# Kernel tuning notes

Measured on AMD Instinct MI355X. Metric: run time of the kernel, lower is better.

The kernel has to match this reference:

```python
import jax, jax.numpy as jnp
import numpy as np

N_NODES = 50000
N_REL = 8
D_IN = 64      # review_dim (in_feats)
D_OUT = 32     # attention_feats (final_dim)
H = 2          # num_heads
N_EDGES = 800000
NEG_SLOPE = 0.2


def gather_mm(x, w, b, idx):
    """Per-edge relation-indexed GEMM: out[e] = x[e] @ w[idx[e]] + b[idx[e]].
    Loops over the small fixed relation set (R=8) instead of materializing
    an [E, D, HF] gathered weight tensor."""
    out = jnp.zeros((x.shape[0], w.shape[-1]), dtype=x.dtype)
    for r in range(w.shape[0]):
        out = out + jnp.where((idx == r)[:, None], x @ w[r] + b[r], jnp.zeros((), x.dtype))
    return out


def setup_inputs() -> dict:
    key = jax.random.key(0)
    ks = jax.random.split(key, 11)
    feat = jax.random.normal(ks[0], (N_NODES, D_IN), dtype=jnp.float32)
    src = jax.random.randint(ks[1], (N_EDGES,), 0, N_NODES)
    dst = jax.random.randint(ks[2], (N_EDGES,), 0, N_NODES)
    r_type = jax.random.randint(ks[3], (N_EDGES,), 0, N_REL)
    nid = jax.random.randint(ks[4], (N_EDGES,), 0, N_NODES)
    fc_src = jax.random.normal(ks[5], (N_REL, D_IN, H * D_OUT), dtype=jnp.float32) * 0.1
    fc_src_bias = jax.random.normal(ks[6], (N_REL, H * D_OUT), dtype=jnp.float32) * 0.1
    node_quality = jax.random.normal(ks[7], (N_NODES, D_IN), dtype=jnp.float32)
    fc_qual = jax.random.normal(ks[8], (N_REL, D_IN, H * D_OUT), dtype=jnp.float32) * 0.1
    fc_qual_bias = jax.random.normal(ks[9], (N_REL, H * D_OUT), dtype=jnp.float32) * 0.1
    attn = jax.random.normal(ks[10], (N_REL, H, D_OUT), dtype=jnp.float32) * 0.1
    return {"feat": feat, "src": src, "dst": dst, "r_type": r_type, "nid": nid,
            "fc_src": fc_src, "fc_src_bias": fc_src_bias, "node_quality": node_quality,
            "fc_qual": fc_qual, "fc_qual_bias": fc_qual_bias, "attn": attn}


def reference(feat, src, dst, r_type, nid, fc_src, fc_src_bias,
              node_quality, fc_qual, fc_qual_bias, attn):
    E = src.shape[0]
    h_src = feat  # feat_drop is identity (p=0)

    # el: relation-aware projection of source features, per edge -> [E, H, D_OUT]
    el = gather_mm(h_src[src], fc_src, fc_src_bias, r_type).reshape(E, H, D_OUT)
    # qual: relation-aware projection of per-edge node-quality embedding
    h_qual = node_quality[nid]
    qual = gather_mm(h_qual, fc_qual, fc_qual_bias, r_type).reshape(E, H, D_OUT)

    # additive attention logits, relation-indexed attn vector -> [E, H]
    e = jax.nn.leaky_relu(el + qual, negative_slope=NEG_SLOPE)
    e = jnp.sum(e * attn[r_type], axis=-1)  # [E, H]

    # edge_softmax over incoming edges of each dst node (per head)
    emax = jax.ops.segment_max(e, dst, num_segments=N_NODES)  # [N, H]
    emax = jnp.where(jnp.isfinite(emax), emax, jnp.zeros((), e.dtype))
    ex = jnp.exp(e - emax[dst])
    denom = jax.ops.segment_sum(ex, dst, num_segments=N_NODES)
    a = ex / denom[dst]  # [E, H]

    # NARRE: messages are raw source features weighted by attention
    msg = h_src[src][:, None, :] * a[:, :, None]  # [E, H, D_IN]
    rst = jax.ops.segment_sum(msg, dst, num_segments=N_NODES)  # [N, H, D_IN]
    return rst
```

## Files before the change

kernel.cpp:

```cpp
#include <hip/hip_runtime.h>
#include <hip/hip_bf16.h>

#define NN 50000
#define NR 8
#define NE 800000
#define NBLK_E 3125
#define NWV (NBLK_E * 4)
#define NCH 13

typedef short bf16x8 __attribute__((ext_vector_type(8)));
typedef float f32x4  __attribute__((ext_vector_type(4)));

__device__ __forceinline__ unsigned fkey(float f) {
    unsigned b = __float_as_uint(f);
    return (b & 0x80000000u) ? ~b : (b | 0x80000000u);
}
__device__ __forceinline__ float funkey(unsigned k) {
    unsigned b = (k & 0x80000000u) ? (k ^ 0x80000000u) : ~k;
    return __uint_as_float(b);
}
__device__ __forceinline__ unsigned short f2bf(float f) {
    unsigned u = __float_as_uint(f);
    unsigned r = (u + 0x7FFFu + ((u >> 16) & 1u)) >> 16;
    return (unsigned short)r;
}
__device__ __forceinline__ float bf2f(unsigned short b) {
    return __uint_as_float(((unsigned)b) << 16);
}

__global__ __launch_bounds__(256) void conv_kernel(
    const float* __restrict__ feat, const float* __restrict__ nq,
    const float* __restrict__ WS, const float* __restrict__ WQ,
    const float* __restrict__ bS, const float* __restrict__ bQ,
    unsigned short* __restrict__ xS, unsigned short* __restrict__ xQ,
    unsigned short* __restrict__ WtS, unsigned short* __restrict__ WtQ,
    float* __restrict__ bSQ)
{
    const int idx = blockIdx.x * 256 + threadIdx.x;
    const int NX = NN * 64 / 4;
    if (idx < NX) {
        const float4 v = reinterpret_cast<const float4*>(feat)[idx];
        ushort4 p; p.x = f2bf(v.x); p.y = f2bf(v.y); p.z = f2bf(v.z); p.w = f2bf(v.w);
        reinterpret_cast<ushort4*>(xS)[idx] = p;
    } else if (idx < 2 * NX) {
        const float4 v = reinterpret_cast<const float4*>(nq)[idx - NX];
        ushort4 p; p.x = f2bf(v.x); p.y = f2bf(v.y); p.z = f2bf(v.z); p.w = f2bf(v.w);
        reinterpret_cast<ushort4*>(xQ)[idx - NX] = p;
    } else {
        int i = idx - 2 * NX;
        if (i < 32768) {
            const int r = i >> 12, rem = i & 4095, o = rem >> 6, k = rem & 63;
            WtS[i] = f2bf(WS[(size_t)r * 4096 + k * 64 + o]);
        } else if (i < 65536) {
            i -= 32768;
            const int r = i >> 12, rem = i & 4095, o = rem >> 6, k = rem & 63;
            WtQ[i] = f2bf(WQ[(size_t)r * 4096 + k * 64 + o]);
        } else if (i < 65536 + 512) {
            const int j = i - 65536;
            bSQ[j] = bS[j] + bQ[j];
        }
    }
}

__global__ __launch_bounds__(256) void hist_kernel(
    const int* __restrict__ dst, const int* __restrict__ rt,
    int* __restrict__ cnt, int* __restrict__ rank, int* __restrict__ rhist)
{
    const int t = threadIdx.x, e = blockIdx.x * 256 + t;
    const int w = t >> 6, lane = t & 63;
    const int d = dst[e], r = rt[e];
    rank[e] = atomicAdd(&cnt[d], 1);
    #pragma unroll
    for (int rr = 0; rr < 8; ++rr) {
        const unsigned long long m = __ballot(r == rr);
        if (lane == 0) rhist[rr * NWV + blockIdx.x * 4 + w] = __popcll(m);
    }
}

__global__ __launch_bounds__(256) void scanrb1_kernel(
    const int* __restrict__ rhist, int* __restrict__ rbase0, int* __restrict__ psum)
{
    __shared__ int s[256];
    __shared__ int carry;
    const int c = blockIdx.x, r = blockIdx.y, t = threadIdx.x;
    if (t == 0) carry = 0;
    __syncthreads();
    const int i1 = min((c + 1) * 1024, NWV);
    for (int b0 = c * 1024; b0 < i1; b0 += 256) {
        const int i = b0 + t;
        const int v = (i < i1) ? rhist[r * NWV + i] : 0;
        s[t] = v;
        __syncthreads();
        #pragma unroll
        for (int off = 1; off < 256; off <<= 1) {
            const int x = (t >= off) ? s[t - off] : 0;
            __syncthreads();
            s[t] += x;
            __syncthreads();
        }
        if (i < i1) rbase0[r * NWV + i] = carry + s[t] - v;
        __syncthreads();
        if (t == 0) carry += s[255];
        __syncthreads();
    }
    if (t == 0) psum[r * NCH + c] = carry;
}

__global__ __launch_bounds__(256) void scan1_kernel(
    const int* __restrict__ cnt, int* __restrict__ offs, int* __restrict__ partial)
{
    __shared__ int s[256];
    const int t = threadIdx.x, i = blockIdx.x * 256 + t;
    const int v = (i < NN) ? cnt[i] : 0;
    s[t] = v;
    __syncthreads();
    #pragma unroll
    for (int off = 1; off < 256; off <<= 1) {
        const int x = (t >= off) ? s[t - off] : 0;
        __syncthreads();
        s[t] += x;
        __syncthreads();
    }
    if (i < NN) offs[i] = s[t] - v;
    if (t == 255) partial[blockIdx.x] = s[255];
}

__global__ __launch_bounds__(256) void scan2_kernel(
    int* __restrict__ partial, const int nblk,
    const int* __restrict__ psum, int* __restrict__ off_pad,
    int* __restrict__ cbase, int4* __restrict__ meta)
{
    __shared__ int s[256];
    __shared__ int sop[9];
    __shared__ int scr[8];
    const int t = threadIdx.x;
    const int v = (t < nblk) ? partial[t] : 0;
    s[t] = v;
    __syncthreads();
    #pragma unroll
    for (int off = 1; off < 256; off <<= 1) {
        const int x = (t >= off) ? s[t - off] : 0;
        __syncthreads();
        s[t] += x;
        __syncthreads();
    }
    if (t < nblk) partial[t] = s[t] - v;
    if (t == 0) {
        int cr[8];
        for (int r = 0; r < NR; ++r) {
            cr[r] = 0;
            for (int c = 0; c < NCH; ++c) cr[r] += psum[r * NCH + c];
        }
        int acc = 0;
        for (int r = 0; r < NR; ++r) {
            sop[r] = acc; off_pad[r] = acc; scr[r] = cr[r];
            int a2 = acc;
            for (int c = 0; c < NCH; ++c) { cbase[r * NCH + c] = a2; a2 += psum[r * NCH + c]; }
            acc += (cr[r] + 255) & ~255;
        }
        sop[8] = acc; off_pad[8] = acc;
    }
    __syncthreads();
    for (int r = 0; r < NR; ++r) {
        const int s0 = sop[r] + scr[r], s1 = sop[r + 1];
        for (int i = s0 + t; i < s1; i += 256) meta[i] = make_int4(0, 0, -1, 0);
    }
}

__global__ __launch_bounds__(256) void scan3_kernel(
    int* __restrict__ offs, const int* __restrict__ partial)
{
    const int i = blockIdx.x * 256 + threadIdx.x;
    if (i < NN) offs[i] += partial[blockIdx.x];
    if (i == 0) offs[NN] = NE;
}

__global__ __launch_bounds__(256) void fillr_kernel(
    const int* __restrict__ rt, const int* __restrict__ src,
    const int* __restrict__ nid, const int* __restrict__ dst,
    const int* __restrict__ offs, const int* __restrict__ rank,
    const int* __restrict__ rbase0, const int* __restrict__ cbase,
    int4* __restrict__ meta)
{
    const int t = threadIdx.x, e = blockIdx.x * 256 + t;
    const int w = t >> 6, lane = t & 63;
    const int r = rt[e];
    unsigned long long mymask = 0;
    #pragma unroll
    for (int rr = 0; rr < 8; ++rr) {
        const unsigned long long m = __ballot(r == rr);
        if (r == rr) mymask = m;
    }
    const int rk = (int)__popcll(mymask & ((1ull << lane) - 1ull));
    const int wv = blockIdx.x * 4 + w;
    const int slot = cbase[r * NCH + (wv >> 10)] + rbase0[r * NWV + wv] + rk;
    const int j = offs[dst[e]] + rank[e];
    meta[slot] = make_int4(src[e], nid[e], j, 0);
}

__global__ __launch_bounds__(256) void logits_kernel(
    const unsigned short* __restrict__ xS, const unsigned short* __restrict__ xQ,
    const unsigned short* __restrict__ WtS, const unsigned short* __restrict__ WtQ,
    const float* __restrict__ bSQ, const float* __restrict__ attn,
    const int4* __restrict__ meta, const int* __restrict__ off_pad,
    float4* __restrict__ perm)
{
    __shared__ bf16x8 ldsS[512];
    __shared__ bf16x8 ldsQ[512];
    const int slot0 = blockIdx.x * 256;
    int r = 0;
    #pragma unroll
    for (int i = 1; i <= 8; ++i) r += (slot0 >= off_pad[i]);
    if (r >= 8) return;

    const int t = threadIdx.x;
    for (int c = t; c < 512; c += 256) {
        const int row = c >> 3, c8 = c & 7, sw = c8 ^ (row & 7);
        ldsS[row * 8 + sw] = *reinterpret_cast<const bf16x8*>(WtS + (size_t)r * 4096 + c * 8);
        ldsQ[row * 8 + sw] = *reinterpret_cast<const bf16x8*>(WtQ + (size_t)r * 4096 + c * 8);
    }
    __syncthreads();

    const int lane = t & 63, l15 = lane & 15, g = lane >> 4, l7 = l15 & 7;
    const int sbase = slot0 + (t >> 6) * 64;

    int4 mt[4];
    #pragma unroll
    for (int b = 0; b < 4; ++b) mt[b] = meta[sbase + b * 16 + l15];

    bf16x8 xf[4][2], qf[4][2];
    #pragma unroll
    for (int b = 0; b < 4; ++b) {
        const unsigned short* xp = xS + (size_t)mt[b].x * 64;
        const unsigned short* qp = xQ + (size_t)mt[b].y * 64;
        xf[b][0] = *reinterpret_cast<const bf16x8*>(xp + g * 8);
        xf[b][1] = *reinterpret_cast<const bf16x8*>(xp + 32 + g * 8);
        qf[b][0] = *reinterpret_cast<const bf16x8*>(qp + g * 8);
        qf[b][1] = *reinterpret_cast<const bf16x8*>(qp + 32 + g * 8);
    }

    float p0[4] = {0.f, 0.f, 0.f, 0.f}, p1[4] = {0.f, 0.f, 0.f, 0.f};
    #pragma unroll
    for (int ot = 0; ot < 4; ++ot) {
        const int row8 = (ot * 16 + l15) * 8;
        const bf16x8 wS0 = ldsS[row8 + (g ^ l7)];
        const bf16x8 wS1 = ldsS[row8 + ((4 + g) ^ l7)];
        const bf16x8 wQ0 = ldsQ[row8 + (g ^ l7)];
        const bf16x8 wQ1 = ldsQ[row8 + ((4 + g) ^ l7)];
        const f32x4 bv = *reinterpret_cast<const f32x4*>(bSQ  + r * 64 + ot * 16 + g * 4);
        const f32x4 av = *reinterpret_cast<const f32x4*>(attn + r * 64 + ot * 16 + g * 4);
        #pragma unroll
        for (int b = 0; b < 4; ++b) {
            f32x4 acc = (f32x4){0.f, 0.f, 0.f, 0.f};
            acc = __builtin_amdgcn_mfma_f32_16x16x32_bf16(wS0, xf[b][0], acc, 0, 0, 0);
            acc = __builtin_amdgcn_mfma_f32_16x16x32_bf16(wS1, xf[b][1], acc, 0, 0, 0);
            acc = __builtin_amdgcn_mfma_f32_16x16x32_bf16(wQ0, qf[b][0], acc, 0, 0, 0);
            acc = __builtin_amdgcn_mfma_f32_16x16x32_bf16(wQ1, qf[b][1], acc, 0, 0, 0);
            float part = 0.f;
            #pragma unroll
            for (int j = 0; j < 4; ++j) {
                float v = acc[j] + bv[j];
                v = v > 0.f ? v : 0.2f * v;
                part += v * av[j];
            }
            if (ot < 2) p0[b] += part; else p1[b] += part;
        }
    }
    #pragma unroll
    for (int b = 0; b < 4; ++b) {
        p0[b] += __shfl_xor(p0[b], 16); p0[b] += __shfl_xor(p0[b], 32);
        p1[b] += __shfl_xor(p1[b], 16); p1[b] += __shfl_xor(p1[b], 32);
        if (g == 0 && mt[b].z >= 0)
            perm[mt[b].z] = make_float4(__int_as_float(mt[b].x), p0[b], p1[b], 0.f);
    }
}

__global__ __launch_bounds__(256) void aggregate_kernel(
    const unsigned short* __restrict__ xS, const int* __restrict__ offs,
    const float4* __restrict__ perm, float* __restrict__ out)
{
    __shared__ float2 ebuf[4][64];
    __shared__ int    sbuf[4][64];
    const int wv = threadIdx.x >> 6;
    const int n = blockIdx.x * 4 + wv;
    if (n >= NN) return;
    const int lane = threadIdx.x & 63;
    const int h2 = lane >> 5;
    const int dp = lane & 31;
    const int s0 = offs[n], s1 = offs[n + 1];
    float a00 = 0.f, a01 = 0.f, a10 = 0.f, a11 = 0.f;
    float d0s = 0.f, d1s = 0.f;
    if (s1 > s0) {
        float m0 = -1e30f, m1 = -1e30f;
        for (int j = s0 + lane; j < s1; j += 64) {
            const float4 p = perm[j];
            m0 = fmaxf(m0, p.y); m1 = fmaxf(m1, p.z);
        }
        #pragma unroll
        for (int m = 32; m; m >>= 1) {
            m0 = fmaxf(m0, __shfl_xor(m0, m));
            m1 = fmaxf(m1, __shfl_xor(m1, m));
        }
        for (int c = s0; c < s1; c += 64) {
            const int cnt = min(64, s1 - c);
            if (lane < cnt) {
                const float4 p = perm[c + lane];
                const float e0 = __expf(p.y - m0);
                const float e1 = __expf(p.z - m1);
                d0s += e0; d1s += e1;
                ebuf[wv][lane] = make_float2(e0, e1);
                sbuf[wv][lane] = (int)__float_as_uint(p.x);
            } else if (lane == cnt) {
                ebuf[wv][lane] = make_float2(0.f, 0.f);
                sbuf[wv][lane] = 0;
            }
            const int cp = cnt + (cnt & 1);
            #pragma unroll 4
            for (int k = 0; k < cp; k += 2) {
                const int ei = k + h2;
                const int sA = sbuf[wv][ei];
                const float2 w = ebuf[wv][ei];
                const unsigned fv = *reinterpret_cast<const unsigned*>(
                    xS + (size_t)sA * 64 + dp * 2);
                const float fx = bf2f((unsigned short)(fv & 0xFFFFu));
                const float fy = bf2f((unsigned short)(fv >> 16));
                a00 += fx * w.x; a01 += fy * w.x;
                a10 += fx * w.y; a11 += fy * w.y;
            }
        }
        #pragma unroll
        for (int m = 32; m; m >>= 1) {
            d0s += __shfl_xor(d0s, m);
            d1s += __shfl_xor(d1s, m);
        }
        a00 += __shfl_xor(a00, 32); a01 += __shfl_xor(a01, 32);
        a10 += __shfl_xor(a10, 32); a11 += __shfl_xor(a11, 32);
        const float r0 = 1.f / d0s, r1 = 1.f / d1s;
        a00 *= r0; a01 *= r0; a10 *= r1; a11 *= r1;
    }
    if (h2 == 0)
        *reinterpret_cast<float2*>(&out[(size_t)n * 128 + dp * 2])      = make_float2(a00, a01);
    else
        *reinterpret_cast<float2*>(&out[(size_t)n * 128 + 64 + dp * 2]) = make_float2(a10, a11);
}

__global__ __launch_bounds__(256) void logits_direct_kernel(
    const float* __restrict__ feat, const float* __restrict__ nq,
    const int* __restrict__ src, const int* __restrict__ dst,
    const int* __restrict__ rt, const int* __restrict__ nid,
    const float* __restrict__ fc_src, const float* __restrict__ fc_src_b,
    const float* __restrict__ fc_qual, const float* __restrict__ fc_qual_b,
    const float* __restrict__ attn,
    float* __restrict__ e_buf, unsigned* __restrict__ emax)
{
    __shared__ float Ws[64][64];
    __shared__ float Wq[64][64];
    __shared__ float bl[64];
    __shared__ float al[64];
    const int r = blockIdx.y;
    const int t = threadIdx.x;
    for (int i = t; i < 4096; i += 256) {
        ((float*)Ws)[i] = fc_src[(size_t)r * 4096 + i];
        ((float*)Wq)[i] = fc_qual[(size_t)r * 4096 + i];
    }
    if (t < 64) {
        bl[t] = fc_src_b[r * 64 + t] + fc_qual_b[r * 64 + t];
        al[t] = attn[r * 64 + t];
    }
    __syncthreads();

    const int lane = t & 63;
    const int wid = blockIdx.x * 4 + (t >> 6);
    const int nw = gridDim.x * 4;
    for (int e = wid; e < NE; e += nw) {
        if (rt[e] != r) continue;
        const int s = src[e], q = nid[e];
        float fv = feat[(size_t)s * 64 + lane];
        float qv = nq[(size_t)q * 64 + lane];
        float acc = bl[lane];
        for (int k = 0; k < 64; ++k) {
            acc += __shfl(fv, k) * Ws[k][lane];
            acc += __shfl(qv, k) * Wq[k][lane];
        }
        acc = acc > 0.f ? acc : 0.2f * acc;
        float p = acc * al[lane];
        #pragma unroll
        for (int m = 1; m < 32; m <<= 1) p += __shfl_xor(p, m);
        if ((lane & 31) == 0) {
            int h = lane >> 5;
            e_buf[(size_t)e * 2 + h] = p;
            atomicMax(&emax[(size_t)dst[e] * 2 + h], fkey(p));
        }
    }
}

__global__ __launch_bounds__(256) void expdenom_kernel(
    const int* __restrict__ dst, float* __restrict__ e_buf,
    const unsigned* __restrict__ emax, float* __restrict__ denom)
{
    const int i = blockIdx.x * 256 + threadIdx.x;
    if (i >= NE * 2) return;
    const int e = i >> 1, h = i & 1;
    const int dn = dst[e];
    const float m = funkey(emax[(size_t)dn * 2 + h]);
    const float ex = __expf(e_buf[i] - m);
    e_buf[i] = ex;
    unsafeAtomicAdd(&denom[(size_t)dn * 2 + h], ex);
}

__global__ __launch_bounds__(256) void scatter_kernel(
    const float* __restrict__ feat, const int* __restrict__ src, const int* __restrict__ dst,
    const float* __restrict__ ex, const float* __restrict__ denom, float* __restrict__ out)
{
    const int e = blockIdx.x * 4 + (threadIdx.x >> 6);
    if (e >= NE) return;
    const int lane = threadIdx.x & 63;
    const int s = src[e], dn = dst[e];
    const float f = feat[(size_t)s * 64 + lane];
    const float a0 = ex[(size_t)e * 2]     / denom[(size_t)dn * 2];
    const float a1 = ex[(size_t)e * 2 + 1] / denom[(size_t)dn * 2 + 1];
    unsafeAtomicAdd(&out[(size_t)dn * 128 + lane],      f * a0);
    unsafeAtomicAdd(&out[(size_t)dn * 128 + 64 + lane], f * a1);
}

extern "C" void kernel_launch(void* const* d_in, const int* in_sizes, int n_in,
                              void* d_out, int out_size, void* d_ws, size_t ws_size,
                              hipStream_t stream)
{
    const float* feat      = (const float*)d_in[0];
    const int*   src       = (const int*)d_in[1];
    const int*   dst       = (const int*)d_in[2];
    const int*   rt        = (const int*)d_in[3];
    const int*   nid       = (const int*)d_in[4];
    const float* fc_src    = (const float*)d_in[5];
    const float* fc_src_b  = (const float*)d_in[6];
    const float* nq        = (const float*)d_in[7];
    const float* fc_qual   = (const float*)d_in[8];
    const float* fc_qual_b = (const float*)d_in[9];
    const float* attn      = (const float*)d_in[10];
    float* out = (float*)d_out;

    char* ws = (char*)d_ws;

    int*    cnt      = (int*)ws;
    int*    offs     = (int*)(ws + 262144);
    int*    partial  = (int*)(ws + 524288);
    int*    off_pad  = (int*)(ws + 528384);
    int*    psum     = (int*)(ws + 528512);
    int*    cbase    = (int*)(ws + 528960);
    int*    rhist    = (int*)(ws + 655360);
    int*    rbase0   = (int*)(ws + 1055360);
    int*    rank     = (int*)(ws + 1455360);
    int4*   meta     = (int4*)(ws + 4718592);
    float4* perm     = (float4*)(ws + 17551360);
    unsigned short* xS  = (unsigned short*)(ws + 30351360);
    unsigned short* xQ  = (unsigned short*)(ws + 36751360);
    unsigned short* WtS = (unsigned short*)(ws + 43151360);
    unsigned short* WtQ = (unsigned short*)(ws + 43216896);
    float*          bSQ = (float*)(ws + 43282432);
    const size_t need = 43284480;

    if (ws_size >= need) {
        hipMemsetAsync(cnt, 0, 200000, stream);

        conv_kernel<<<6508, 256, 0, stream>>>(
            feat, nq, fc_src, fc_qual, fc_src_b, fc_qual_b, xS, xQ, WtS, WtQ, bSQ);
        hist_kernel<<<NBLK_E, 256, 0, stream>>>(dst, rt, cnt, rank, rhist);
        {
            dim3 g(NCH, NR);
            scanrb1_kernel<<<g, 256, 0, stream>>>(rhist, rbase0, psum);
        }

        const int nblk = (NN + 255) / 256;
        scan1_kernel<<<nblk, 256, 0, stream>>>(cnt, offs, partial);
        scan2_kernel<<<1, 256, 0, stream>>>(partial, nblk, psum, off_pad, cbase, meta);
        scan3_kernel<<<nblk, 256, 0, stream>>>(offs, partial);
        fillr_kernel<<<NBLK_E, 256, 0, stream>>>(
            rt, src, nid, dst, offs, rank, rbase0, cbase, meta);

        logits_kernel<<<(NE + 8 * 256) / 256, 256, 0, stream>>>(
            xS, xQ, WtS, WtQ, bSQ, attn, meta, off_pad, perm);
        aggregate_kernel<<<(NN + 3) / 4, 256, 0, stream>>>(xS, offs, perm, out);
    } else {
        float*    e_buf = (float*)ws;
        unsigned* emax  = (unsigned*)(ws + (size_t)NE * 2 * 4);
        float*    denom = (float*)(ws + (size_t)NE * 2 * 4 + (size_t)NN * 2 * 4);
        hipMemsetAsync(out, 0, (size_t)out_size * sizeof(float), stream);
        hipMemsetAsync(emax, 0, (size_t)NN * 2 * 4 * 2, stream);
        dim3 g(256, NR);
        logits_direct_kernel<<<g, 256, 0, stream>>>(
            feat, nq, src, dst, rt, nid, fc_src, fc_src_b, fc_qual, fc_qual_b,
            attn, e_buf, emax);
        expdenom_kernel<<<(NE * 2 + 255) / 256, 256, 0, stream>>>(dst, e_buf, emax, denom);
        scatter_kernel<<<(NE + 3) / 4, 256, 0, stream>>>(feat, src, dst, e_buf, denom, out);
    }
}
```

Measured before the change: 160.8 us.

## Fuse conversion with histogram, compress logits to bf16, prefetch weights to registers

Merges the bf16 conversion kernel and the dst/relation histogram kernel into one launch, removing a kernel launch and its gap. The per-edge logits record shrinks from a float4 to a uint2 holding the source index plus two bf16-packed logits, halving perm traffic between the logits and aggregate kernels. In the logits kernel, weight tiles are loaded into registers before the gathers and written to LDS afterwards, so global weight loads overlap the feature gathers. Storing logits in bf16 lowers softmax precision and may affect accuracy.

```diff
diff --git a/kernel.cpp b/kernel.cpp
--- a/kernel.cpp
+++ b/kernel.cpp
@@ -28,15 +28,19 @@
     return __uint_as_float(((unsigned)b) << 16);
 }
 
-__global__ __launch_bounds__(256) void conv_kernel(
+__global__ __launch_bounds__(256) void conv_hist_kernel(
     const float* __restrict__ feat, const float* __restrict__ nq,
     const float* __restrict__ WS, const float* __restrict__ WQ,
     const float* __restrict__ bS, const float* __restrict__ bQ,
+    const int* __restrict__ dst, const int* __restrict__ rt,
     unsigned short* __restrict__ xS, unsigned short* __restrict__ xQ,
     unsigned short* __restrict__ WtS, unsigned short* __restrict__ WtQ,
-    float* __restrict__ bSQ)
-{
-    const int idx = blockIdx.x * 256 + threadIdx.x;
+    float* __restrict__ bSQ,
+    int* __restrict__ cnt, int* __restrict__ rank, int* __restrict__ rhist)
+{
+    const int t = threadIdx.x;
+    const int idx = blockIdx.x * 256 + t;
+
     const int NX = NN * 64 / 4;
     if (idx < NX) {
         const float4 v = reinterpret_cast<const float4*>(feat)[idx];
@@ -60,20 +64,16 @@
             bSQ[j] = bS[j] + bQ[j];
         }
     }
-}
-
-__global__ __launch_bounds__(256) void hist_kernel(
-    const int* __restrict__ dst, const int* __restrict__ rt,
-    int* __restrict__ cnt, int* __restrict__ rank, int* __restrict__ rhist)
-{
-    const int t = threadIdx.x, e = blockIdx.x * 256 + t;
-    const int w = t >> 6, lane = t & 63;
-    const int d = dst[e], r = rt[e];
-    rank[e] = atomicAdd(&cnt[d], 1);
-    #pragma unroll
-    for (int rr = 0; rr < 8; ++rr) {
-        const unsigned long long m = __ballot(r == rr);
-        if (lane == 0) rhist[rr * NWV + blockIdx.x * 4 + w] = __popcll(m);
+
+    if (blockIdx.x < NBLK_E) {
+        const int w = t >> 6, lane = t & 63;
+        const int d = dst[idx], r = rt[idx];
+        rank[idx] = atomicAdd(&cnt[d], 1);
+        #pragma unroll
+        for (int rr = 0; rr < 8; ++rr) {
+            const unsigned long long m = __ballot(r == rr);
+            if (lane == 0) rhist[rr * NWV + blockIdx.x * 4 + w] = __popcll(m);
+        }
     }
 }
 
@@ -203,7 +203,7 @@
     const unsigned short* __restrict__ WtS, const unsigned short* __restrict__ WtQ,
     const float* __restrict__ bSQ, const float* __restrict__ attn,
     const int4* __restrict__ meta, const int* __restrict__ off_pad,
-    float4* __restrict__ perm)
+    uint2* __restrict__ perm)
 {
     __shared__ bf16x8 ldsS[512];
     __shared__ bf16x8 ldsQ[512];
@@ -214,20 +214,20 @@
     if (r >= 8) return;
 
     const int t = threadIdx.x;
-    for (int c = t; c < 512; c += 256) {
-        const int row = c >> 3, c8 = c & 7, sw = c8 ^ (row & 7);
-        ldsS[row * 8 + sw] = *reinterpret_cast<const bf16x8*>(WtS + (size_t)r * 4096 + c * 8);
-        ldsQ[row * 8 + sw] = *reinterpret_cast<const bf16x8*>(WtQ + (size_t)r * 4096 + c * 8);
-    }
-    __syncthreads();
-
     const int lane = t & 63, l15 = lane & 15, g = lane >> 4, l7 = l15 & 7;
     const int sbase = slot0 + (t >> 6) * 64;
 
+    bf16x8 wrS[2], wrQ[2];
+    #pragma unroll
+    for (int i = 0; i < 2; ++i) {
+        const int c = t + i * 256;
+        wrS[i] = *reinterpret_cast<const bf16x8*>(WtS + (size_t)r * 4096 + c * 8);
+        wrQ[i] = *reinterpret_cast<const bf16x8*>(WtQ + (size_t)r * 4096 + c * 8);
+    }
+
     int4 mt[4];
     #pragma unroll
     for (int b = 0; b < 4; ++b) mt[b] = meta[sbase + b * 16 + l15];
-
     bf16x8 xf[4][2], qf[4][2];
     #pragma unroll
     for (int b = 0; b < 4; ++b) {
@@ -238,6 +238,15 @@
         qf[b][0] = *reinterpret_cast<const bf16x8*>(qp + g * 8);
         qf[b][1] = *reinterpret_cast<const bf16x8*>(qp + 32 + g * 8);
     }
+
+    #pragma unroll
+    for (int i = 0; i < 2; ++i) {
+        const int c = t + i * 256;
+        const int row = c >> 3, c8 = c & 7, sw = c8 ^ (row & 7);
+        ldsS[row * 8 + sw] = wrS[i];
+        ldsQ[row * 8 + sw] = wrQ[i];
+    }
+    __syncthreads();
 
     float p0[4] = {0.f, 0.f, 0.f, 0.f}, p1[4] = {0.f, 0.f, 0.f, 0.f};
     #pragma unroll
@@ -270,14 +279,16 @@
     for (int b = 0; b < 4; ++b) {
         p0[b] += __shfl_xor(p0[b], 16); p0[b] += __shfl_xor(p0[b], 32);
         p1[b] += __shfl_xor(p1[b], 16); p1[b] += __shfl_xor(p1[b], 32);
-        if (g == 0 && mt[b].z >= 0)
-            perm[mt[b].z] = make_float4(__int_as_float(mt[b].x), p0[b], p1[b], 0.f);
+        if (g == 0 && mt[b].z >= 0) {
+            const unsigned pk = ((unsigned)f2bf(p0[b]) << 16) | (unsigned)f2bf(p1[b]);
+            perm[mt[b].z] = make_uint2((unsigned)mt[b].x, pk);
+        }
     }
 }
 
 __global__ __launch_bounds__(256) void aggregate_kernel(
     const unsigned short* __restrict__ xS, const int* __restrict__ offs,
-    const float4* __restrict__ perm, float* __restrict__ out)
+    const uint2* __restrict__ perm, float* __restrict__ out)
 {
     __shared__ float2 ebuf[4][64];
     __shared__ int    sbuf[4][64];
@@ -293,8 +304,9 @@
     if (s1 > s0) {
         float m0 = -1e30f, m1 = -1e30f;
         for (int j = s0 + lane; j < s1; j += 64) {
-            const float4 p = perm[j];
-            m0 = fmaxf(m0, p.y); m1 = fmaxf(m1, p.z);
+            const uint2 p = perm[j];
+            m0 = fmaxf(m0, bf2f((unsigned short)(p.y >> 16)));
+            m1 = fmaxf(m1, bf2f((unsigned short)(p.y & 0xFFFFu)));
         }
         #pragma unroll
         for (int m = 32; m; m >>= 1) {
@@ -304,12 +316,12 @@
         for (int c = s0; c < s1; c += 64) {
             const int cnt = min(64, s1 - c);
             if (lane < cnt) {
-                const float4 p = perm[c + lane];
-                const float e0 = __expf(p.y - m0);
-                const float e1 = __expf(p.z - m1);
+                const uint2 p = perm[c + lane];
+                const float e0 = __expf(bf2f((unsigned short)(p.y >> 16)) - m0);
+                const float e1 = __expf(bf2f((unsigned short)(p.y & 0xFFFFu)) - m1);
                 d0s += e0; d1s += e1;
                 ebuf[wv][lane] = make_float2(e0, e1);
-                sbuf[wv][lane] = (int)__float_as_uint(p.x);
+                sbuf[wv][lane] = (int)p.x;
             } else if (lane == cnt) {
                 ebuf[wv][lane] = make_float2(0.f, 0.f);
                 sbuf[wv][lane] = 0;
@@ -452,7 +464,7 @@
     int*    rbase0   = (int*)(ws + 1055360);
     int*    rank     = (int*)(ws + 1455360);
     int4*   meta     = (int4*)(ws + 4718592);
-    float4* perm     = (float4*)(ws + 17551360);
+    uint2*  perm     = (uint2*)(ws + 17551360);
     unsigned short* xS  = (unsigned short*)(ws + 30351360);
     unsigned short* xQ  = (unsigned short*)(ws + 36751360);
     unsigned short* WtS = (unsigned short*)(ws + 43151360);
@@ -463,9 +475,9 @@
     if (ws_size >= need) {
         hipMemsetAsync(cnt, 0, 200000, stream);
 
-        conv_kernel<<<6508, 256, 0, stream>>>(
-            feat, nq, fc_src, fc_qual, fc_src_b, fc_qual_b, xS, xQ, WtS, WtQ, bSQ);
-        hist_kernel<<<NBLK_E, 256, 0, stream>>>(dst, rt, cnt, rank, rhist);
+        conv_hist_kernel<<<6508, 256, 0, stream>>>(
+            feat, nq, fc_src, fc_qual, fc_src_b, fc_qual_b, dst, rt,
+            xS, xQ, WtS, WtQ, bSQ, cnt, rank, rhist);
         {
             dim3 g(NCH, NR);
             scanrb1_kernel<<<g, 256, 0, stream>>>(rhist, rbase0, psum);
```

New measurement: 150.4 us. 1.07x faster.
